# Kernel optimization log

Measured on AMD Instinct MI355X. Metric: run time of the kernel, lower is better.

The kernel has to match this reference:

```python
import jax, jax.numpy as jnp
import numpy as np

B, N, H, EMB, BOT = 32, 128, 64, 64, 64


def _node2edge(x):
    # x: (B, N, F) -> edges (B, N*N, 2F); edge e=i*N+j holds [x[j] (receiver), x[i] (sender)]
    b, n, f = x.shape
    recv = jnp.broadcast_to(x[:, None, :, :], (b, n, n, f))  # varies with j
    send = jnp.broadcast_to(x[:, :, None, :], (b, n, n, f))  # varies with i
    return jnp.concatenate([recv, send], axis=-1).reshape(b, n * n, 2 * f)


def _edge2node(e, n):
    # e: (B, N*N, F); receiver of edge i*N+j is j -> sum over i; divide by FEATURE dim (faithful to source)
    b, _, f = e.shape
    return e.reshape(b, n, n, f).sum(axis=1) / f


def _lin(x, w, b):
    return x @ w + b


def setup_inputs() -> dict:
    key = jax.random.key(0)
    ks = jax.random.split(key, 24)

    def w(k, i, o):
        return jax.random.normal(k, (i, o), jnp.float32) / np.sqrt(i)

    def bias(k, o):
        return jax.random.normal(k, (o,), jnp.float32) * 0.01

    return {
        "h_states": jax.random.normal(ks[0], (B, N, H), jnp.float32),
        "end_pos": jax.random.normal(ks[1], (B, N, 2), jnp.float32),
        "se_w": w(ks[2], 2, EMB), "se_b": bias(ks[3], EMB),
        "s1_w": w(ks[4], 2 * H + EMB, 128), "s1_b": bias(ks[5], 128),
        "s2_w": w(ks[6], 128, H), "s2_b": bias(ks[7], H),
        "n1_w": w(ks[8], H, 128), "n1_b": bias(ks[9], 128),
        "n2_w": w(ks[10], 128, H), "n2_b": bias(ks[11], H),
        "e1_w": w(ks[12], 2 * H, 128), "e1_b": bias(ks[13], 128),
        "e2_w": w(ks[14], 128, H), "e2_b": bias(ks[15], H),
        "f1_w": w(ks[16], H, 128), "f1_b": bias(ks[17], 128),
        "f2_w": w(ks[18], 128, BOT), "f2_b": bias(ks[19], BOT),
    }


def reference(h_states, end_pos, se_w, se_b, s1_w, s1_b, s2_w, s2_b,
              n1_w, n1_b, n2_w, n2_b, e1_w, e1_b, e2_w, e2_b,
              f1_w, f1_b, f2_w, f2_b):
    b, n, _ = h_states.shape
    # relative positions: pos[i] - pos[j] for edge i*N+j -> (B, N*N, 2)
    rel_pos = (end_pos[:, :, None, :] - end_pos[:, None, :, :]).reshape(b, n * n, 2)
    rel_emb = _lin(rel_pos, se_w, se_b)  # (B, N*N, EMB)

    edge_feat = jnp.concatenate([_node2edge(h_states), rel_emb], axis=-1)  # (B, N*N, 2H+EMB)
    # nmp_mlp_start: two linears, no activation (activation=None), dropout inert in eval
    edge_feat = _lin(_lin(edge_feat, s1_w, s1_b), s2_w, s2_b)  # (B, N*N, H)

    # nmp_layers=2 -> one (node mlp, edge mlp) pair, no activations
    node_feat = _lin(_lin(_edge2node(edge_feat, n), n1_w, n1_b), n2_w, n2_b)
    edge_feat = _lin(_lin(_node2edge(node_feat), e1_w, e1_b), e2_w, e2_b)

    # nmp_mlp_end: Linear -> ReLU -> Linear -> ReLU
    x = _edge2node(edge_feat, n)
    x = jax.nn.relu(_lin(x, f1_w, f1_b))
    x = jax.nn.relu(_lin(x, f2_w, f2_b))
    return x  # (B, N, BOT)
```

## Files before the change

### kernel.cpp

```cpp
#include <hip/hip_runtime.h>

enum : int {
  WS_H1 = 0,
  WS_H2 = 8192,
  WS_H3 = 8448,
  WS_END = 12544
};

__global__ __launch_bounds__(256) void k_prep(
    const float* __restrict__ h, const float* __restrict__ pos,
    const float* __restrict__ se_w, const float* __restrict__ se_b,
    const float* __restrict__ s1_w, const float* __restrict__ s1_b,
    const float* __restrict__ s2_w, const float* __restrict__ s2_b,
    const float* __restrict__ n1_w, const float* __restrict__ n1_b,
    const float* __restrict__ n2_w, const float* __restrict__ n2_b,
    const float* __restrict__ e1_w, const float* __restrict__ e1_b,
    const float* __restrict__ e2_w, const float* __restrict__ e2_b,
    const float* __restrict__ f1_w, const float* __restrict__ f1_b,
    float* __restrict__ ws)
{
  __shared__ __align__(16) float smem[9472];
  int blk = blockIdx.x, t = threadIdx.x;

  if (blk < 64) {
    float* W  = smem;
    float* VA = smem + 8320;
    float* VB = smem + 8704;
    float* PT = smem + 9088;
    const int c0 = blk * 2;
    const int j = t & 1, rb = t >> 1;

    #define STAGE_W_128x64(ptr) \
      { _Pragma("unroll") for (int it = 0; it < 8; ++it) { \
          int i = t + it * 256; int row = i >> 4, col = (i & 15) * 4; \
          *(float4*)&W[row * 65 + col] = *(const float4*)((ptr) + row * 64 + col); } }
    #define STAGE_W_64x128(ptr) \
      { _Pragma("unroll") for (int it = 0; it < 8; ++it) { \
          int i = t + it * 256; int row = i >> 5, col = (i & 31) * 4; \
          *(float4*)&W[row * 129 + col] = *(const float4*)((ptr) + row * 128 + col); } }
    #define MUL_128x64(IN, OUT) \
      { float a0=0.f,a1=0.f,a2=0.f,a3=0.f; \
        _Pragma("unroll") for (int k = 0; k < 16; ++k) { \
          a0 = fmaf(W[rb*65 + k],      IN[(k)*3 + j],      a0); \
          a1 = fmaf(W[rb*65 + 16 + k], IN[(16 + k)*3 + j], a1); \
          a2 = fmaf(W[rb*65 + 32 + k], IN[(32 + k)*3 + j], a2); \
          a3 = fmaf(W[rb*65 + 48 + k], IN[(48 + k)*3 + j], a3); } \
        OUT[rb*3 + j] = (a0 + a1) + (a2 + a3); }
    #define MUL_64x128_PART(IN) \
      { float a0=0.f,a1=0.f,a2=0.f,a3=0.f; int r = rb & 63, kb = (rb >> 6) * 64; \
        _Pragma("unroll") for (int k = 0; k < 16; ++k) { \
          a0 = fmaf(W[r*129 + kb + k],      IN[(kb + k)*3 + j],      a0); \
          a1 = fmaf(W[r*129 + kb + 16 + k], IN[(kb + 16 + k)*3 + j], a1); \
          a2 = fmaf(W[r*129 + kb + 32 + k], IN[(kb + 32 + k)*3 + j], a2); \
          a3 = fmaf(W[r*129 + kb + 48 + k], IN[(kb + 48 + k)*3 + j], a3); } \
        PT[rb*3 + j] = (a0 + a1) + (a2 + a3); }

    if (t < 128) { int k = t >> 1; VA[k * 3 + (t & 1)] = f1_w[k * 128 + c0 + (t & 1)]; }
    STAGE_W_128x64(e2_w);
    __syncthreads();
    MUL_128x64(VA, VB);
    __syncthreads();
    STAGE_W_64x128(e1_w);
    __syncthreads();
    MUL_64x128_PART(VB);
    __syncthreads();
    if (rb < 64) VA[rb * 3 + j] = PT[rb * 3 + j] + PT[(rb + 64) * 3 + j];
    STAGE_W_128x64(n2_w);
    __syncthreads();
    MUL_128x64(VA, VB);
    __syncthreads();
    STAGE_W_64x128(n1_w);
    __syncthreads();
    MUL_64x128_PART(VB);
    __syncthreads();
    if (rb < 64) VA[rb * 3 + j] = PT[rb * 3 + j] + PT[(rb + 64) * 3 + j];
    STAGE_W_128x64(s2_w);
    __syncthreads();
    MUL_128x64(VA, VB);
    __syncthreads();
    STAGE_W_64x128(s1_w);
    __syncthreads();
    MUL_64x128_PART(VB);
    __syncthreads();
    if (rb < 64)
      ws[WS_H1 + rb * 128 + c0 + j] = 4.f * (PT[rb * 3 + j] + PT[(rb + 64) * 3 + j]);
    STAGE_W_64x128(s1_w + 128 * 128);
    __syncthreads();
    MUL_64x128_PART(VB);
    __syncthreads();
    if (rb < 64) VA[rb * 3 + j] = PT[rb * 3 + j] + PT[(rb + 64) * 3 + j];
    __syncthreads();
    if (t < 4) {
      int r2 = t >> 1, jj = t & 1;
      float a0 = 0.f, a1 = 0.f, a2 = 0.f, a3 = 0.f;
      #pragma unroll
      for (int k = 0; k < 16; ++k) {
        a0 = fmaf(se_w[r2 * 64 + k],      VA[(k) * 3 + jj],      a0);
        a1 = fmaf(se_w[r2 * 64 + 16 + k], VA[(16 + k) * 3 + jj], a1);
        a2 = fmaf(se_w[r2 * 64 + 32 + k], VA[(32 + k) * 3 + jj], a2);
        a3 = fmaf(se_w[r2 * 64 + 48 + k], VA[(48 + k) * 3 + jj], a3);
      }
      ws[WS_H2 + r2 * 128 + c0 + jj] = -4.f * ((a0 + a1) + (a2 + a3));
    }
    #undef STAGE_W_128x64
    #undef STAGE_W_64x128
    #undef MUL_128x64
    #undef MUL_64x128_PART
  } else {
    int b = blk - 64;
    float* part = smem;
    float* sX = smem + 256;
    float* sP = smem + 320;
    float* L0 = smem + 384;
    float* L1 = smem + 512;
    float* L2 = smem + 640;
    float* L3 = smem + 768;
    float* M0 = smem + 896;
    float* M1 = smem + 960;
    { int k = t & 63, g = t >> 6; float s = 0.f;
      #pragma unroll 8
      for (int jn = g * 32; jn < g * 32 + 32; ++jn) s += h[(b * 128 + jn) * 64 + k];
      part[t] = s; }
    __syncthreads();
    if (t < 64) sX[t] = (part[t] + part[64 + t]) + (part[128 + t] + part[192 + t]);
    else if (t < 128) {
      int l = t - 64;
      const float* pb = pos + b * 256;
      float s = (pb[l] + pb[64 + l]) + (pb[128 + l] + pb[192 + l]);
      #pragma unroll
      for (int m = 2; m <= 32; m <<= 1) s += __shfl_xor(s, m, 64);
      if (l < 2) sP[l] = s;
    }
    __syncthreads();
    { int g = t >> 7, o = t & 127;
      if (g == 0) {
        float a0 = 0.f, a1 = 0.f, k0 = 0.f, k1 = 0.f;
        #pragma unroll
        for (int k = 0; k < 32; ++k) {
          a0 = fmaf(sX[k],        s1_w[k * 128 + o],                a0);
          a1 = fmaf(sX[32 + k],   s1_w[(32 + k) * 128 + o],         a1);
          k0 = fmaf(se_b[k],      s1_w[(128 + k) * 128 + o],        k0);
          k1 = fmaf(se_b[32 + k], s1_w[(160 + k) * 128 + o],        k1);
        }
        L0[o] = a0 + a1; L1[o] = (k0 + k1) + s1_b[o];
      } else {
        float p0 = sP[0], p1 = sP[1];
        float a0 = 0.f, a1 = 0.f, y0 = 0.f, y1 = 0.f;
        #pragma unroll
        for (int k = 0; k < 32; ++k) {
          a0 = fmaf(sX[k],      s1_w[(64 + k) * 128 + o], a0);
          a1 = fmaf(sX[32 + k], s1_w[(96 + k) * 128 + o], a1);
          float qa = fmaf(p1, se_w[64 + k], p0 * se_w[k]);
          float qb = fmaf(p1, se_w[96 + k], p0 * se_w[32 + k]);
          y0 = fmaf(qa, s1_w[(128 + k) * 128 + o], y0);
          y1 = fmaf(qb, s1_w[(160 + k) * 128 + o], y1);
        }
        L2[o] = a0 + a1; L3[o] = y0 + y1;
      } }
    __syncthreads();
    if (t < 128) { int g = t >> 6, c = t & 63;
      float a0 = 0.f, a1 = 0.f;
      if (g == 0) {
        #pragma unroll
        for (int o = 0; o < 64; ++o) {
          float ra = fmaf(2.f, L1[o],      (L2[o] + L3[o]) * (1.f / 64.f));
          float rb2 = fmaf(2.f, L1[64 + o], (L2[64 + o] + L3[64 + o]) * (1.f / 64.f));
          a0 = fmaf(ra,  s2_w[o * 64 + c],        a0);
          a1 = fmaf(rb2, s2_w[(64 + o) * 64 + c], a1);
        }
        M0[c] = (a0 + a1) + 2.f * s2_b[c];
      } else {
        #pragma unroll
        for (int o = 0; o < 64; ++o) {
          a0 = fmaf(2.f * (L0[o] - L3[o]),           s2_w[o * 64 + c],        a0);
          a1 = fmaf(2.f * (L0[64 + o] - L3[64 + o]), s2_w[(64 + o) * 64 + c], a1);
        }
        M1[c] = a0 + a1;
      } }
    __syncthreads();
    { int g = t >> 7, o = t & 127;
      float a0 = 0.f, a1 = 0.f;
      const float* mv = (g == 0) ? M0 : M1;
      #pragma unroll
      for (int k = 0; k < 32; ++k) {
        a0 = fmaf(mv[k],      n1_w[k * 128 + o],        a0);
        a1 = fmaf(mv[32 + k], n1_w[(32 + k) * 128 + o], a1);
      }
      if (g == 0) L0[o] = (a0 + a1) + n1_b[o]; else L1[o] = a0 + a1; }
    __syncthreads();
    if (t < 128) { int g = t >> 6, c = t & 63;
      const float* lv = (g == 0) ? L0 : L1;
      float a0 = 0.f, a1 = 0.f;
      #pragma unroll
      for (int o = 0; o < 64; ++o) {
        a0 = fmaf(lv[o],      n2_w[o * 64 + c],        a0);
        a1 = fmaf(lv[64 + o], n2_w[(64 + o) * 64 + c], a1);
      }
      if (g == 0) M0[c] = (a0 + a1) + n2_b[c]; else M1[c] = a0 + a1; }
    __syncthreads();
    { int g = t >> 7, o = t & 127;
      float a0 = 0.f, a1 = 0.f;
      if (g == 0) {
        #pragma unroll
        for (int k = 0; k < 32; ++k) {
          a0 = fmaf(M0[k],      e1_w[k * 128 + o],        a0);
          a1 = fmaf(M0[32 + k], e1_w[(32 + k) * 128 + o], a1);
        }
        L0[o] = a0 + a1;
      } else {
        #pragma unroll
        for (int k = 0; k < 32; ++k) {
          float na = fmaf(128.f, M0[k],      M1[k]);
          float nb = fmaf(128.f, M0[32 + k], M1[32 + k]);
          a0 = fmaf(na, e1_w[(64 + k) * 128 + o], a0);
          a1 = fmaf(nb, e1_w[(96 + k) * 128 + o], a1);
        }
        L1[o] = a0 + a1;
      } }
    __syncthreads();
    if (t < 64) { float a0 = 0.f, a1 = 0.f;
      #pragma unroll
      for (int o = 0; o < 64; ++o) {
        float ga = fmaf(L1[o],      (1.f / 64.f), fmaf(2.f, L0[o],      2.f * e1_b[o]));
        float gb = fmaf(L1[64 + o], (1.f / 64.f), fmaf(2.f, L0[64 + o], 2.f * e1_b[64 + o]));
        a0 = fmaf(ga, e2_w[o * 64 + t],        a0);
        a1 = fmaf(gb, e2_w[(64 + o) * 64 + t], a1);
      }
      M0[t] = (a0 + a1) + 2.f * e2_b[t]; }
    __syncthreads();
    if (t < 128) { float a0 = 0.f, a1 = 0.f;
      #pragma unroll
      for (int k = 0; k < 32; ++k) {
        a0 = fmaf(M0[k],      f1_w[k * 128 + t],        a0);
        a1 = fmaf(M0[32 + k], f1_w[(32 + k) * 128 + t], a1);
      }
      ws[WS_H3 + b * 128 + t] = (a0 + a1) + f1_b[t]; }
  }
}

__global__ __launch_bounds__(256) void k_main(
    const float* __restrict__ h, const float* __restrict__ pos,
    const float* __restrict__ f2_w, const float* __restrict__ f2_b,
    const float* __restrict__ ws, float* __restrict__ out)
{
  __shared__ __align__(16) float lH1[64 * 128];
  __shared__ __align__(16) float lx[16 * 64];
  __shared__ float lp[16 * 2];
  __shared__ __align__(16) float lh1[16 * 128];
  int blk = blockIdx.x, t = threadIdx.x;
  int b = blk >> 3, j0 = (blk & 7) * 16;
  for (int i = t; i < 2048; i += 256) ((float4*)lH1)[i] = ((const float4*)(ws + WS_H1))[i];
  ((float4*)lx)[t] = ((const float4*)(h + (size_t)(b * 128 + j0) * 64))[t];
  if (t < 32) lp[t] = pos[(b * 128 + j0) * 2 + t];
  __syncthreads();
  {
    int d = t & 127, g = t >> 7, n0 = g * 8;
    float h3v = ws[WS_H3 + b * 128 + d];
    float h2a = ws[WS_H2 + d], h2b = ws[WS_H2 + 128 + d];
    float acc[8];
    #pragma unroll
    for (int i = 0; i < 8; ++i)
      acc[i] = h3v + lp[(n0 + i) * 2] * h2a + lp[(n0 + i) * 2 + 1] * h2b;
    #pragma unroll 4
    for (int k = 0; k < 64; k += 4) {
      float h0 = lH1[k * 128 + d], h1v = lH1[(k + 1) * 128 + d],
            h2v = lH1[(k + 2) * 128 + d], h3w = lH1[(k + 3) * 128 + d];
      #pragma unroll
      for (int i = 0; i < 8; ++i) {
        float4 xv = *(const float4*)&lx[(n0 + i) * 64 + k];
        acc[i] = fmaf(xv.x, h0, fmaf(xv.y, h1v, fmaf(xv.z, h2v, fmaf(xv.w, h3w, acc[i]))));
      }
    }
    #pragma unroll
    for (int i = 0; i < 8; ++i) lh1[(n0 + i) * 128 + d] = fmaxf(acc[i], 0.f);
  }
  __syncthreads();
  {
    int d = t & 63, g = t >> 6, n0 = g * 4;
    float acc[4];
    float bias = f2_b[d];
    #pragma unroll
    for (int i = 0; i < 4; ++i) acc[i] = bias;
    #pragma unroll 4
    for (int k = 0; k < 128; k += 4) {
      float f0 = f2_w[k * 64 + d], f1v = f2_w[(k + 1) * 64 + d],
            f2v = f2_w[(k + 2) * 64 + d], f3v = f2_w[(k + 3) * 64 + d];
      #pragma unroll
      for (int i = 0; i < 4; ++i) {
        float4 hv = *(const float4*)&lh1[(n0 + i) * 128 + k];
        acc[i] = fmaf(hv.x, f0, fmaf(hv.y, f1v, fmaf(hv.z, f2v, fmaf(hv.w, f3v, acc[i]))));
      }
    }
    #pragma unroll
    for (int i = 0; i < 4; ++i)
      out[(size_t)(b * 128 + j0 + n0 + i) * 64 + d] = fmaxf(acc[i], 0.f);
  }
}

extern "C" void kernel_launch(void* const* d_in, const int* in_sizes, int n_in,
                              void* d_out, int out_size, void* d_ws, size_t ws_size,
                              hipStream_t stream) {
  const float* h    = (const float*)d_in[0];
  const float* pos  = (const float*)d_in[1];
  const float* se_w = (const float*)d_in[2];
  const float* se_b = (const float*)d_in[3];
  const float* s1_w = (const float*)d_in[4];
  const float* s1_b = (const float*)d_in[5];
  const float* s2_w = (const float*)d_in[6];
  const float* s2_b = (const float*)d_in[7];
  const float* n1_w = (const float*)d_in[8];
  const float* n1_b = (const float*)d_in[9];
  const float* n2_w = (const float*)d_in[10];
  const float* n2_b = (const float*)d_in[11];
  const float* e1_w = (const float*)d_in[12];
  const float* e1_b = (const float*)d_in[13];
  const float* e2_w = (const float*)d_in[14];
  const float* e2_b = (const float*)d_in[15];
  const float* f1_w = (const float*)d_in[16];
  const float* f1_b = (const float*)d_in[17];
  const float* f2_w = (const float*)d_in[18];
  const float* f2_b = (const float*)d_in[19];
  float* ws = (float*)d_ws;
  float* out = (float*)d_out;

  hipLaunchKernelGGL(k_prep, dim3(96), dim3(256), 0, stream,
                     h, pos, se_w, se_b, s1_w, s1_b, s2_w, s2_b,
                     n1_w, n1_b, n2_w, n2_b, e1_w, e1_b, e2_w, e2_b,
                     f1_w, f1_b, ws);
  hipLaunchKernelGGL(k_main, dim3(256), dim3(256), 0, stream, h, pos, f2_w, f2_b, ws, out);
}
```

Before: 29.71 us.

## Compute weight-chain products in forward order, skipping shared-memory weight staging

```diff
diff --git a/kernel.cpp b/kernel.cpp
--- a/kernel.cpp
+++ b/kernel.cpp
@@ -19,95 +19,68 @@
     const float* __restrict__ f1_w, const float* __restrict__ f1_b,
     float* __restrict__ ws)
 {
-  __shared__ __align__(16) float smem[9472];
+  __shared__ __align__(16) float smem[1024];
   int blk = blockIdx.x, t = threadIdx.x;
 
-  if (blk < 64) {
-    float* W  = smem;
-    float* VA = smem + 8320;
-    float* VB = smem + 8704;
-    float* PT = smem + 9088;
-    const int c0 = blk * 2;
-    const int j = t & 1, rb = t >> 1;
-
-    #define STAGE_W_128x64(ptr) \
-      { _Pragma("unroll") for (int it = 0; it < 8; ++it) { \
-          int i = t + it * 256; int row = i >> 4, col = (i & 15) * 4; \
-          *(float4*)&W[row * 65 + col] = *(const float4*)((ptr) + row * 64 + col); } }
-    #define STAGE_W_64x128(ptr) \
-      { _Pragma("unroll") for (int it = 0; it < 8; ++it) { \
-          int i = t + it * 256; int row = i >> 5, col = (i & 31) * 4; \
-          *(float4*)&W[row * 129 + col] = *(const float4*)((ptr) + row * 128 + col); } }
-    #define MUL_128x64(IN, OUT) \
-      { float a0=0.f,a1=0.f,a2=0.f,a3=0.f; \
-        _Pragma("unroll") for (int k = 0; k < 16; ++k) { \
-          a0 = fmaf(W[rb*65 + k],      IN[(k)*3 + j],      a0); \
-          a1 = fmaf(W[rb*65 + 16 + k], IN[(16 + k)*3 + j], a1); \
-          a2 = fmaf(W[rb*65 + 32 + k], IN[(32 + k)*3 + j], a2); \
-          a3 = fmaf(W[rb*65 + 48 + k], IN[(48 + k)*3 + j], a3); } \
-        OUT[rb*3 + j] = (a0 + a1) + (a2 + a3); }
-    #define MUL_64x128_PART(IN) \
-      { float a0=0.f,a1=0.f,a2=0.f,a3=0.f; int r = rb & 63, kb = (rb >> 6) * 64; \
-        _Pragma("unroll") for (int k = 0; k < 16; ++k) { \
-          a0 = fmaf(W[r*129 + kb + k],      IN[(kb + k)*3 + j],      a0); \
-          a1 = fmaf(W[r*129 + kb + 16 + k], IN[(kb + 16 + k)*3 + j], a1); \
-          a2 = fmaf(W[r*129 + kb + 32 + k], IN[(kb + 32 + k)*3 + j], a2); \
-          a3 = fmaf(W[r*129 + kb + 48 + k], IN[(kb + 48 + k)*3 + j], a3); } \
-        PT[rb*3 + j] = (a0 + a1) + (a2 + a3); }
-
-    if (t < 128) { int k = t >> 1; VA[k * 3 + (t & 1)] = f1_w[k * 128 + c0 + (t & 1)]; }
-    STAGE_W_128x64(e2_w);
-    __syncthreads();
-    MUL_128x64(VA, VB);
-    __syncthreads();
-    STAGE_W_64x128(e1_w);
-    __syncthreads();
-    MUL_64x128_PART(VB);
-    __syncthreads();
-    if (rb < 64) VA[rb * 3 + j] = PT[rb * 3 + j] + PT[(rb + 64) * 3 + j];
-    STAGE_W_128x64(n2_w);
-    __syncthreads();
-    MUL_128x64(VA, VB);
-    __syncthreads();
-    STAGE_W_64x128(n1_w);
-    __syncthreads();
-    MUL_64x128_PART(VB);
-    __syncthreads();
-    if (rb < 64) VA[rb * 3 + j] = PT[rb * 3 + j] + PT[(rb + 64) * 3 + j];
-    STAGE_W_128x64(s2_w);
-    __syncthreads();
-    MUL_128x64(VA, VB);
-    __syncthreads();
-    STAGE_W_64x128(s1_w);
-    __syncthreads();
-    MUL_64x128_PART(VB);
-    __syncthreads();
-    if (rb < 64)
-      ws[WS_H1 + rb * 128 + c0 + j] = 4.f * (PT[rb * 3 + j] + PT[(rb + 64) * 3 + j]);
-    STAGE_W_64x128(s1_w + 128 * 128);
-    __syncthreads();
-    MUL_64x128_PART(VB);
-    __syncthreads();
-    if (rb < 64) VA[rb * 3 + j] = PT[rb * 3 + j] + PT[(rb + 64) * 3 + j];
-    __syncthreads();
-    if (t < 4) {
-      int r2 = t >> 1, jj = t & 1;
-      float a0 = 0.f, a1 = 0.f, a2 = 0.f, a3 = 0.f;
-      #pragma unroll
-      for (int k = 0; k < 16; ++k) {
-        a0 = fmaf(se_w[r2 * 64 + k],      VA[(k) * 3 + jj],      a0);
-        a1 = fmaf(se_w[r2 * 64 + 16 + k], VA[(16 + k) * 3 + jj], a1);
-        a2 = fmaf(se_w[r2 * 64 + 32 + k], VA[(32 + k) * 3 + jj], a2);
-        a3 = fmaf(se_w[r2 * 64 + 48 + k], VA[(48 + k) * 3 + jj], a3);
-      }
-      ws[WS_H2 + r2 * 128 + c0 + jj] = -4.f * ((a0 + a1) + (a2 + a3));
-    }
-    #undef STAGE_W_128x64
-    #undef STAGE_W_64x128
-    #undef MUL_128x64
-    #undef MUL_64x128_PART
+  if (blk < 33) {
+    float (*v128)[128] = (float(*)[128])smem;
+    float (*v64)[64]   = (float(*)[64])(smem + 256);
+    float (*pt)[2][64] = (float(*)[2][64])(smem + 384);
+    const int row = t >> 7;
+    const int c128 = t & 127;
+    const int c64 = t & 63;
+    const int half = (t >> 6) & 1;
+
+    if (blk == 32) {
+      float a0 = 0.f, a1 = 0.f;
+      #pragma unroll
+      for (int k = 0; k < 32; ++k) {
+        a0 = fmaf(se_w[row * 64 + k],      s1_w[(128 + k) * 128 + c128], a0);
+        a1 = fmaf(se_w[row * 64 + 32 + k], s1_w[(160 + k) * 128 + c128], a1);
+      }
+      v128[row][c128] = a0 + a1;
+    } else {
+      v128[row][c128] = s1_w[(blk * 2 + row) * 128 + c128];
+    }
+    __syncthreads();
+
+    #define STAGE_DN(W) \
+      { float a0 = 0.f, a1 = 0.f; \
+        _Pragma("unroll") for (int k = 0; k < 32; ++k) { \
+          a0 = fmaf(v128[row][half * 64 + k],      (W)[(half * 64 + k) * 64 + c64],      a0); \
+          a1 = fmaf(v128[row][half * 64 + 32 + k], (W)[(half * 64 + 32 + k) * 64 + c64], a1); } \
+        pt[row][half][c64] = a0 + a1; } \
+      __syncthreads(); \
+      if (t < 128) v64[t >> 6][t & 63] = pt[t >> 6][0][t & 63] + pt[t >> 6][1][t & 63]; \
+      __syncthreads();
+
+    #define STAGE_UP(W) \
+      { float a0 = 0.f, a1 = 0.f; \
+        _Pragma("unroll") for (int k = 0; k < 32; ++k) { \
+          a0 = fmaf(v64[row][k],      (W)[k * 128 + c128],        a0); \
+          a1 = fmaf(v64[row][32 + k], (W)[(32 + k) * 128 + c128], a1); } \
+        v128[row][c128] = a0 + a1; } \
+      __syncthreads();
+
+    STAGE_DN(s2_w)
+    STAGE_UP(n1_w)
+    STAGE_DN(n2_w)
+    STAGE_UP(e1_w)
+    STAGE_DN(e2_w)
+    { float a0 = 0.f, a1 = 0.f;
+      #pragma unroll
+      for (int k = 0; k < 32; ++k) {
+        a0 = fmaf(v64[row][k],      f1_w[k * 128 + c128],        a0);
+        a1 = fmaf(v64[row][32 + k], f1_w[(32 + k) * 128 + c128], a1);
+      }
+      float r = a0 + a1;
+      if (blk == 32) ws[WS_H2 + row * 128 + c128] = -4.f * r;
+      else           ws[WS_H1 + (blk * 2 + row) * 128 + c128] = 4.f * r;
+    }
+    #undef STAGE_DN
+    #undef STAGE_UP
   } else {
-    int b = blk - 64;
+    int b = blk - 33;
     float* part = smem;
     float* sX = smem + 256;
     float* sP = smem + 320;
@@ -137,10 +110,10 @@
         float a0 = 0.f, a1 = 0.f, k0 = 0.f, k1 = 0.f;
         #pragma unroll
         for (int k = 0; k < 32; ++k) {
-          a0 = fmaf(sX[k],        s1_w[k * 128 + o],                a0);
-          a1 = fmaf(sX[32 + k],   s1_w[(32 + k) * 128 + o],         a1);
-          k0 = fmaf(se_b[k],      s1_w[(128 + k) * 128 + o],        k0);
-          k1 = fmaf(se_b[32 + k], s1_w[(160 + k) * 128 + o],        k1);
+          a0 = fmaf(sX[k],        s1_w[k * 128 + o],         a0);
+          a1 = fmaf(sX[32 + k],   s1_w[(32 + k) * 128 + o],  a1);
+          k0 = fmaf(se_b[k],      s1_w[(128 + k) * 128 + o], k0);
+          k1 = fmaf(se_b[32 + k], s1_w[(160 + k) * 128 + o], k1);
         }
         L0[o] = a0 + a1; L1[o] = (k0 + k1) + s1_b[o];
       } else {
@@ -163,7 +136,7 @@
       if (g == 0) {
         #pragma unroll
         for (int o = 0; o < 64; ++o) {
-          float ra = fmaf(2.f, L1[o],      (L2[o] + L3[o]) * (1.f / 64.f));
+          float ra  = fmaf(2.f, L1[o],      (L2[o] + L3[o]) * (1.f / 64.f));
           float rb2 = fmaf(2.f, L1[64 + o], (L2[64 + o] + L3[64 + o]) * (1.f / 64.f));
           a0 = fmaf(ra,  s2_w[o * 64 + c],        a0);
           a1 = fmaf(rb2, s2_w[(64 + o) * 64 + c], a1);
@@ -323,7 +296,7 @@
   float* ws = (float*)d_ws;
   float* out = (float*)d_out;
 
-  hipLaunchKernelGGL(k_prep, dim3(96), dim3(256), 0, stream,
+  hipLaunchKernelGGL(k_prep, dim3(65), dim3(256), 0, stream,
                      h, pos, se_w, se_b, s1_w, s1_b, s2_w, s2_b,
                      n1_w, n1_b, n2_w, n2_b, e1_w, e1_b, e2_w, e2_b,
                      f1_w, f1_b, ws);
```

New measurement: 29.59 us. Within noise of the previous version (-0.4%).
